# Optimization experiments

Hardware: AMD Instinct MI355X
Metric: run time of the kernel (lower is better)

Reference implementation:

```python
import jax, jax.numpy as jnp
import numpy as np

B, T, C = 4, 4096, 1024
NH, DH = 16, 128          # n_head, d_head = d_qkv // n_head
DQKV, DR = 2048, 256      # d_qkv, d_rank


def _uniform(key, shape, bound):
    return jax.random.uniform(key, shape, jnp.float32, -bound, bound)


def setup_inputs() -> dict:
    key = jax.random.key(0)
    k0, k1, k2, k3, k4 = jax.random.split(key, 5)
    # CastedLinear init: bound = sqrt(3) * 0.5 * in_features**-0.5 (same for w1, w2)
    b_qkv = (3 ** 0.5) * 0.5 * C ** (-0.5)
    b_proj = (3 ** 0.5) * 0.5 * DQKV ** (-0.5)
    return {
        "x": jax.random.normal(k0, (B, T, C), jnp.float32),
        "qkv_w1": _uniform(k1, (DR, C), b_qkv),
        "qkv_w2": _uniform(k2, (3 * DQKV, DR), b_qkv),
        "cproj_w1": _uniform(k3, (DR, DQKV), b_proj),
        "cproj_w2": _uniform(k4, (2 * C, DR), b_proj),
    }


def _rmsnorm(x):
    eps = jnp.finfo(x.dtype).eps  # F.rms_norm default eps
    return x * jax.lax.rsqrt(jnp.mean(x * x, axis=-1, keepdims=True) + eps)


def reference(x, qkv_w1, qkv_w2, cproj_w1, cproj_w2):
    Bx, Tx, Cx = x.shape
    # qkv projection with low-rank factorization + relu^2 activation between factors
    h = _rmsnorm(x) @ qkv_w1.T                      # [B,T,DR]
    h = jnp.square(jax.nn.relu(h))
    qkv = (h @ qkv_w2.T).reshape(Bx, Tx, 3 * NH, DH)
    q, k, v = jnp.split(qkv, 3, axis=2)             # each [B,T,NH,DH]
    q, k = _rmsnorm(q), _rmsnorm(k)

    # rotary embedding: half the head dim rotated, second quarter frequencies zero
    quarter = DH // 4
    freq = (1.0 / 1024.0) ** jnp.linspace(0.0, 1.0, quarter)
    freq = jnp.concatenate([freq, jnp.zeros(quarter, freq.dtype)])  # [DH//2]
    theta = jnp.arange(Tx, dtype=jnp.float32)[:, None] * freq[None, :]
    cos = jnp.cos(theta)[None, :, None, :]          # [1,T,1,DH//2]
    sin = jnp.sin(theta)[None, :, None, :]

    def rope(z):
        z1, z2 = jnp.split(z, 2, axis=-1)
        return jnp.concatenate([z1 * cos + z2 * sin, -z1 * sin + z2 * cos], axis=-1)

    q, k = rope(q), rope(k)

    # causal linear attention: sigmoid-gated cumulative sum over time
    y = jax.nn.relu(q) * jnp.cumsum(jax.nn.sigmoid(k) * v, axis=1)  # [B,T,NH,DH]
    y = y.reshape(Bx, Tx, NH * DH)

    # low-rank output projection (no activation), gated residual
    uv = (y @ cproj_w1.T) @ cproj_w2.T              # [B,T,2C]
    u, g = jnp.split(uv, 2, axis=-1)
    return x + u * jax.nn.silu(g)
```

## Files before the change

### kernel.cpp

```cpp
#include <hip/hip_runtime.h>
#include <hip/hip_bf16.h>

#define TB 4
#define TT 4096
#define TC 1024
#define TNH 16
#define TDH 128
#define TDQKV 2048
#define TDR 256
#define RB 4096
#define ROWS (TB*TT)
#define SLAB (RB*128)
#define NSEG 128
#define SEGT 32

typedef __attribute__((ext_vector_type(8))) short bfx8;
typedef __attribute__((ext_vector_type(4))) float fx4;
typedef __attribute__((address_space(1))) const unsigned char GAS;
typedef __attribute__((address_space(3))) unsigned char LAS;

__device__ __forceinline__ unsigned short f2b(float f) {
    unsigned int u = __float_as_uint(f);
    unsigned int r = (u + 0x7fffu + ((u >> 16) & 1u)) >> 16;
    return (unsigned short)r;
}
__device__ __forceinline__ float b2f(unsigned short h) {
    return __uint_as_float(((unsigned int)h) << 16);
}
__device__ __forceinline__ float sigm(float x) {
    return 1.0f / (1.0f + __expf(-x));
}
__device__ __forceinline__ int xcd_swz(int hw, int nwg) {
    int q = nwg >> 3;
    return (hw & 7) * q + (hw >> 3);
}

__global__ __launch_bounds__(256) void setup_all(const float* __restrict__ wq1, unsigned short* __restrict__ w1b,
                                                 const float* __restrict__ wq2, unsigned short* __restrict__ w2b,
                                                 const float* __restrict__ wc1, unsigned short* __restrict__ wp1b,
                                                 const float* __restrict__ wc2, unsigned short* __restrict__ wp2b,
                                                 float* __restrict__ ct, float* __restrict__ st) {
    int blk = blockIdx.x;
    if (blk < 2816) {
        const float* in; unsigned short* out; int base;
        if (blk < 256)       { in = wq1; out = w1b;  base = blk; }
        else if (blk < 1792) { in = wq2; out = w2b;  base = blk - 256; }
        else if (blk < 2304) { in = wc1; out = wp1b; base = blk - 1792; }
        else                 { in = wc2; out = wp2b; base = blk - 2304; }
        int i = (base * 256 + threadIdx.x) * 4;
        float4 v = *(const float4*)(in + i);
        out[i + 0] = f2b(v.x);
        out[i + 1] = f2b(v.y);
        out[i + 2] = f2b(v.z);
        out[i + 3] = f2b(v.w);
    } else {
        int i = (blk - 2816) * 256 + threadIdx.x;
        int t = i >> 5, j = i & 31;
        float fr = exp2f(-10.0f * (float)j / 31.0f);
        float th = (float)t * fr;
        ct[i] = cosf(th);
        st[i] = sinf(th);
    }
}

__global__ __launch_bounds__(256) void rmsnorm_x(const float* __restrict__ x,
                                                 unsigned short* __restrict__ xn) {
    int row = blockIdx.x;
    int tid = threadIdx.x;
    float4 v = *(const float4*)(x + (size_t)row * TC + tid * 4);
    float ss = v.x * v.x + v.y * v.y + v.z * v.z + v.w * v.w;
    #pragma unroll
    for (int o = 32; o > 0; o >>= 1) ss += __shfl_xor(ss, o);
    __shared__ float red[4];
    if ((tid & 63) == 0) red[tid >> 6] = ss;
    __syncthreads();
    float tot = red[0] + red[1] + red[2] + red[3];
    float sc = rsqrtf(tot * (1.0f / TC) + 1.1920929e-7f);
    unsigned short* o = xn + (size_t)row * TC + tid * 4;
    o[0] = f2b(v.x * sc); o[1] = f2b(v.y * sc); o[2] = f2b(v.z * sc); o[3] = f2b(v.w * sc);
}

template <int EPI>
__global__ __launch_bounds__(256) void gemm_bt(const unsigned short* __restrict__ A, int lda,
                                               const unsigned short* __restrict__ Bm,
                                               unsigned short* __restrict__ C, int ldc,
                                               int N, int K) {
    __shared__ unsigned short As[2][128 * 32];
    __shared__ unsigned short Bs[2][128 * 32];
    const int m0 = blockIdx.y * 128;
    const int n0 = blockIdx.x * 128;
    const int tid = threadIdx.x;
    const int lane = tid & 63;
    const int w = tid >> 6;
    const int wr = w >> 1, wc = w & 1;
    const int r16 = lane & 15;
    const int kk = (lane >> 4) * 8;
    const int l4 = lane >> 2;
    const int c8 = (lane & 3) * 8;
    const int nk = K >> 5;
    fx4 acc[4][4] = {};

    auto stage = [&](int buf, int k0) {
        #pragma unroll
        for (int i = 0; i < 2; ++i) {
            int rr = (w + 4 * i) * 16 + l4;
            const unsigned short* ga = A + (size_t)(m0 + rr) * lda + k0 + c8;
            const unsigned short* gb = Bm + (size_t)(n0 + rr) * K + k0 + c8;
            __builtin_amdgcn_global_load_lds((GAS*)ga, (LAS*)&As[buf][(w + 4 * i) * 512], 16, 0, 0);
            __builtin_amdgcn_global_load_lds((GAS*)gb, (LAS*)&Bs[buf][(w + 4 * i) * 512], 16, 0, 0);
        }
    };

    stage(0, 0);
    __syncthreads();
    int buf = 0;
    for (int ks = 0; ks < nk; ++ks) {
        if (ks + 1 < nk) stage(buf ^ 1, (ks + 1) * 32);
        bfx8 af[4], bfr[4];
        #pragma unroll
        for (int mi = 0; mi < 4; mi++) af[mi] = *(const bfx8*)&As[buf][(wr * 64 + mi * 16 + r16) * 32 + kk];
        #pragma unroll
        for (int ni = 0; ni < 4; ni++) bfr[ni] = *(const bfx8*)&Bs[buf][(wc * 64 + ni * 16 + r16) * 32 + kk];
        #pragma unroll
        for (int mi = 0; mi < 4; mi++)
            #pragma unroll
            for (int ni = 0; ni < 4; ni++)
                acc[mi][ni] = __builtin_amdgcn_mfma_f32_16x16x32_bf16(af[mi], bfr[ni], acc[mi][ni], 0, 0, 0);
        __syncthreads();
        buf ^= 1;
    }

    const int rg = lane >> 4;
    #pragma unroll
    for (int mi = 0; mi < 4; mi++)
        #pragma unroll
        for (int ni = 0; ni < 4; ni++) {
            int col = n0 + wc * 64 + ni * 16 + r16;
            #pragma unroll
            for (int r = 0; r < 4; r++) {
                int row = m0 + wr * 64 + mi * 16 + rg * 4 + r;
                float v = acc[mi][ni][r];
                if (EPI == 1) { v = fmaxf(v, 0.0f); v *= v; }
                if (EPI == 2) {
                    int head = col >> 7;
                    C[(size_t)head * SLAB + (size_t)row * 128 + (col & 127)] = f2b(v);
                } else {
                    C[(size_t)row * ldc + col] = f2b(v);
                }
            }
        }
}

template <int EPI, int NX>
__global__ __launch_bounds__(256) void gemm_sk(const unsigned short* __restrict__ A, int lda,
                                               const unsigned short* __restrict__ Bm,
                                               unsigned short* __restrict__ C, int ldc,
                                               int K) {
    __shared__ unsigned short As[2][128 * 32];
    __shared__ unsigned short Bs[2][64 * 32];
    const int lg = xcd_swz(blockIdx.x, gridDim.x);
    const int n0 = (lg % NX) * 64;
    const int m0 = (lg / NX) * 128;
    const int tid = threadIdx.x;
    const int lane = tid & 63;
    const int w = tid >> 6;
    const int wr = w >> 1, wc = w & 1;
    const int r16 = lane & 15;
    const int kk = (lane >> 4) * 8;
    const int l4 = lane >> 2;
    const int c8 = (lane & 3) * 8;
    const int nk = K >> 5;
    fx4 acc[4][2] = {};

    auto stage = [&](int buf, int k0) {
        #pragma unroll
        for (int i = 0; i < 2; ++i) {
            int rr = (w + 4 * i) * 16 + l4;
            const unsigned short* ga = A + (size_t)(m0 + rr) * lda + k0 + c8;
            __builtin_amdgcn_global_load_lds((GAS*)ga, (LAS*)&As[buf][(w + 4 * i) * 512], 16, 0, 0);
        }
        const unsigned short* gb = Bm + (size_t)(n0 + w * 16 + l4) * K + k0 + c8;
        __builtin_amdgcn_global_load_lds((GAS*)gb, (LAS*)&Bs[buf][w * 512], 16, 0, 0);
    };

    stage(0, 0);
    __syncthreads();
    int buf = 0;
    for (int ks = 0; ks < nk; ++ks) {
        if (ks + 1 < nk) stage(buf ^ 1, (ks + 1) * 32);
        bfx8 af[4], bfr[2];
        #pragma unroll
        for (int mi = 0; mi < 4; mi++) af[mi] = *(const bfx8*)&As[buf][(wr * 64 + mi * 16 + r16) * 32 + kk];
        #pragma unroll
        for (int ni = 0; ni < 2; ni++) bfr[ni] = *(const bfx8*)&Bs[buf][(wc * 32 + ni * 16 + r16) * 32 + kk];
        #pragma unroll
        for (int mi = 0; mi < 4; mi++)
            #pragma unroll
            for (int ni = 0; ni < 2; ni++)
                acc[mi][ni] = __builtin_amdgcn_mfma_f32_16x16x32_bf16(af[mi], bfr[ni], acc[mi][ni], 0, 0, 0);
        __syncthreads();
        buf ^= 1;
    }

    const int rg = lane >> 4;
    #pragma unroll
    for (int mi = 0; mi < 4; mi++)
        #pragma unroll
        for (int ni = 0; ni < 2; ni++) {
            int col = n0 + wc * 32 + ni * 16 + r16;
            #pragma unroll
            for (int r = 0; r < 4; r++) {
                int row = m0 + wr * 64 + mi * 16 + rg * 4 + r;
                float v = acc[mi][ni][r];
                if (EPI == 1) { v = fmaxf(v, 0.0f); v *= v; }
                C[(size_t)row * ldc + col] = f2b(v);
            }
        }
}

__global__ __launch_bounds__(256) void gemm4f64(const unsigned short* __restrict__ A,
                                                const unsigned short* __restrict__ Wm,
                                                const float* __restrict__ x,
                                                float* __restrict__ out) {
    __shared__ unsigned short As[2][64 * 32];
    __shared__ unsigned short Bu[2][64 * 32];
    __shared__ unsigned short Bg[2][64 * 32];
    const int hw = blockIdx.y * gridDim.x + blockIdx.x;
    const int lg = xcd_swz(hw, gridDim.x * gridDim.y);
    const int n0 = (lg & 15) * 64;
    const int m0 = (lg >> 4) * 64;
    const int tid = threadIdx.x;
    const int lane = tid & 63;
    const int w = tid >> 6;
    const int wr = w >> 1, wc = w & 1;
    const int r16 = lane & 15;
    const int rg = lane >> 4;
    const int kk = rg * 8;
    const int l4 = lane >> 2;
    const int c8 = (lane & 3) * 8;
    fx4 accu[2][2] = {};
    fx4 accg[2][2] = {};

    auto stage = [&](int buf, int k0) {
        int rr = w * 16 + l4;
        const unsigned short* ga = A + (size_t)(m0 + rr) * TDR + k0 + c8;
        const unsigned short* gu = Wm + (size_t)(n0 + rr) * TDR + k0 + c8;
        const unsigned short* gg = Wm + (size_t)(1024 + n0 + rr) * TDR + k0 + c8;
        __builtin_amdgcn_global_load_lds((GAS*)ga, (LAS*)&As[buf][w * 512], 16, 0, 0);
        __builtin_amdgcn_global_load_lds((GAS*)gu, (LAS*)&Bu[buf][w * 512], 16, 0, 0);
        __builtin_amdgcn_global_load_lds((GAS*)gg, (LAS*)&Bg[buf][w * 512], 16, 0, 0);
    };

    stage(0, 0);
    float xr[2][2][4];
    #pragma unroll
    for (int mi = 0; mi < 2; mi++)
        #pragma unroll
        for (int ni = 0; ni < 2; ni++)
            #pragma unroll
            for (int r = 0; r < 4; r++)
                xr[mi][ni][r] = x[(size_t)(m0 + wr * 32 + mi * 16 + rg * 4 + r) * TC
                                  + n0 + wc * 32 + ni * 16 + r16];
    __syncthreads();
    int buf = 0;
    for (int ks = 0; ks < 8; ++ks) {
        if (ks + 1 < 8) stage(buf ^ 1, (ks + 1) * 32);
        bfx8 af[2], bu[2], bg[2];
        #pragma unroll
        for (int mi = 0; mi < 2; mi++) af[mi] = *(const bfx8*)&As[buf][(wr * 32 + mi * 16 + r16) * 32 + kk];
        #pragma unroll
        for (int ni = 0; ni < 2; ni++) {
            bu[ni] = *(const bfx8*)&Bu[buf][(wc * 32 + ni * 16 + r16) * 32 + kk];
            bg[ni] = *(const bfx8*)&Bg[buf][(wc * 32 + ni * 16 + r16) * 32 + kk];
        }
        #pragma unroll
        for (int mi = 0; mi < 2; mi++)
            #pragma unroll
            for (int ni = 0; ni < 2; ni++) {
                accu[mi][ni] = __builtin_amdgcn_mfma_f32_16x16x32_bf16(af[mi], bu[ni], accu[mi][ni], 0, 0, 0);
                accg[mi][ni] = __builtin_amdgcn_mfma_f32_16x16x32_bf16(af[mi], bg[ni], accg[mi][ni], 0, 0, 0);
            }
        __syncthreads();
        buf ^= 1;
    }

    #pragma unroll
    for (int mi = 0; mi < 2; mi++)
        #pragma unroll
        for (int ni = 0; ni < 2; ni++) {
            int col = n0 + wc * 32 + ni * 16 + r16;
            #pragma unroll
            for (int r = 0; r < 4; r++) {
                int row = m0 + wr * 32 + mi * 16 + rg * 4 + r;
                float u = accu[mi][ni][r];
                float g = accg[mi][ni][r];
                out[(size_t)row * TC + col] = xr[mi][ni][r] + u * (g * sigm(g));
            }
        }
}

__global__ __launch_bounds__(256) void post64(unsigned short* __restrict__ qkv,
                                              const float* __restrict__ ct,
                                              const float* __restrict__ st,
                                              float* __restrict__ part) {
    const int blk = blockIdx.x;
    const int tile = blk & 63, h = blk >> 6;
    const int g = threadIdx.x >> 4, l16 = threadIdx.x & 15;
    const int d0 = l16 * 4;
    unsigned short* qs = qkv + (size_t)h * SLAB;
    unsigned short* ks = qkv + (size_t)(16 + h) * SLAB;
    unsigned short* vs = qkv + (size_t)(32 + h) * SLAB;
    __shared__ float psum[2][16][128];
    float acc0[2][4] = {};
    float acc1[2][4] = {};

    #pragma unroll
    for (int p = 0; p < 4; ++p) {
        const int t = tile * 64 + p * 16 + g;
        const size_t lo = (size_t)t * 128 + d0, hi = lo + 64;
        ushort4 q1 = *(const ushort4*)(qs + lo);
        ushort4 q2 = *(const ushort4*)(qs + hi);
        ushort4 k1 = *(const ushort4*)(ks + lo);
        ushort4 k2 = *(const ushort4*)(ks + hi);
        float qa[8] = {b2f(q1.x), b2f(q1.y), b2f(q1.z), b2f(q1.w),
                       b2f(q2.x), b2f(q2.y), b2f(q2.z), b2f(q2.w)};
        float ka[8] = {b2f(k1.x), b2f(k1.y), b2f(k1.z), b2f(k1.w),
                       b2f(k2.x), b2f(k2.y), b2f(k2.z), b2f(k2.w)};
        float ssq = 0.0f, ssk = 0.0f;
        #pragma unroll
        for (int j = 0; j < 8; ++j) { ssq += qa[j] * qa[j]; ssk += ka[j] * ka[j]; }
        #pragma unroll
        for (int o = 8; o > 0; o >>= 1) {
            ssq += __shfl_xor(ssq, o);
            ssk += __shfl_xor(ssk, o);
        }
        float qsc = rsqrtf(ssq * (1.0f / TDH) + 1.1920929e-7f);
        float ksc = rsqrtf(ssk * (1.0f / TDH) + 1.1920929e-7f);
        float c[4], s[4];
        if (l16 < 8) {
            float4 cv = *(const float4*)(ct + t * 32 + d0);
            float4 sv = *(const float4*)(st + t * 32 + d0);
            c[0] = cv.x; c[1] = cv.y; c[2] = cv.z; c[3] = cv.w;
            s[0] = sv.x; s[1] = sv.y; s[2] = sv.z; s[3] = sv.w;
        } else {
            c[0] = c[1] = c[2] = c[3] = 1.0f;
            s[0] = s[1] = s[2] = s[3] = 0.0f;
        }
        ushort4 v1 = *(const ushort4*)(vs + lo);
        ushort4 v2 = *(const ushort4*)(vs + hi);
        float va[8] = {b2f(v1.x), b2f(v1.y), b2f(v1.z), b2f(v1.w),
                       b2f(v2.x), b2f(v2.y), b2f(v2.z), b2f(v2.w)};
        ushort4 qo1, qo2, po1, po2;
        unsigned short* qo1p = (unsigned short*)&qo1;
        unsigned short* qo2p = (unsigned short*)&qo2;
        unsigned short* po1p = (unsigned short*)&po1;
        unsigned short* po2p = (unsigned short*)&po2;
        const int h2 = p >> 1;
        #pragma unroll
        for (int j = 0; j < 4; ++j) {
            float z1q = qa[j] * qsc, z2q = qa[4 + j] * qsc;
            float z1k = ka[j] * ksc, z2k = ka[4 + j] * ksc;
            float qlo = z1q * c[j] + z2q * s[j];
            float qhi = z2q * c[j] - z1q * s[j];
            float klo = z1k * c[j] + z2k * s[j];
            float khi = z2k * c[j] - z1k * s[j];
            float plo = sigm(klo) * va[j];
            float phi = sigm(khi) * va[4 + j];
            qo1p[j] = f2b(qlo); qo2p[j] = f2b(qhi);
            po1p[j] = f2b(plo); po2p[j] = f2b(phi);
            acc0[h2][j] += plo;
            acc1[h2][j] += phi;
        }
        *(ushort4*)(qs + lo) = qo1;
        *(ushort4*)(qs + hi) = qo2;
        *(ushort4*)(ks + lo) = po1;
        *(ushort4*)(ks + hi) = po2;
    }
    #pragma unroll
    for (int h2 = 0; h2 < 2; ++h2) {
        *(float4*)&psum[h2][g][d0]      = *(float4*)acc0[h2];
        *(float4*)&psum[h2][g][64 + d0] = *(float4*)acc1[h2];
    }
    __syncthreads();
    const int h2 = threadIdx.x >> 7, d = threadIdx.x & 127;
    float tot = 0.0f;
    #pragma unroll
    for (int gg = 0; gg < 16; ++gg) tot += psum[h2][gg][d];
    part[((size_t)h * NSEG + tile * 2 + h2) * 128 + d] = tot;
}

__global__ __launch_bounds__(256) void scanB128(float* __restrict__ part) {
    int idx = blockIdx.x * 256 + threadIdx.x;
    int h = idx >> 7, d = idx & 127;
    float run = 0.0f;
    #pragma unroll 8
    for (int s = 0; s < NSEG; ++s) {
        float* p = part + ((size_t)(h * NSEG + s)) * 128 + d;
        float tv = *p;
        *p = run;
        run += tv;
    }
}

__global__ __launch_bounds__(256) void scanC3(const unsigned short* __restrict__ qkv,
                                              const float* __restrict__ part,
                                              unsigned short* __restrict__ y) {
    const int bseg = blockIdx.x & 7, h = blockIdx.x >> 3;
    const int g = threadIdx.x >> 4, l16 = threadIdx.x & 15;
    const int seg = bseg * 16 + g;
    const int d0 = l16 * 8;
    const unsigned short* qp = qkv + (size_t)h * SLAB;
    const unsigned short* pp = qkv + (size_t)(16 + h) * SLAB;
    float sum[8];
    const float* pb = part + ((size_t)(h * NSEG + seg)) * 128 + d0;
    *(float4*)&sum[0] = *(const float4*)pb;
    *(float4*)&sum[4] = *(const float4*)(pb + 4);
    #pragma unroll 4
    for (int i = 0; i < SEGT; ++i) {
        int t = seg * SEGT + i;
        size_t off = (size_t)t * 128 + d0;
        bfx8 pv = *(const bfx8*)(pp + off);
        bfx8 qv = *(const bfx8*)(qp + off);
        bfx8 ov;
        #pragma unroll
        for (int j = 0; j < 8; ++j) {
            sum[j] += b2f((unsigned short)pv[j]);
            float q = b2f((unsigned short)qv[j]);
            ov[j] = (short)f2b(fmaxf(q, 0.0f) * sum[j]);
        }
        *(bfx8*)(y + (size_t)t * 2048 + h * 128 + d0) = ov;
    }
}

extern "C" void kernel_launch(void* const* d_in, const int* in_sizes, int n_in,
                              void* d_out, int out_size, void* d_ws, size_t ws_size,
                              hipStream_t stream) {
    (void)in_sizes; (void)n_in; (void)out_size; (void)ws_size;
    const float* x    = (const float*)d_in[0];
    const float* wq1  = (const float*)d_in[1];
    const float* wq2  = (const float*)d_in[2];
    const float* wc1  = (const float*)d_in[3];
    const float* wc2  = (const float*)d_in[4];
    float* out = (float*)d_out;

    char* ws = (char*)d_ws;
    size_t off = 0;
    auto alloc = [&](size_t bytes) -> void* {
        off = (off + 255) & ~(size_t)255;
        void* p = ws + off;
        off += bytes;
        return p;
    };
    char* pool = (char*)alloc((size_t)RB * 6144 * 2);
    unsigned short* qkvb = (unsigned short*)pool;
    unsigned short* xn   = (unsigned short*)pool;
    unsigned short* t1   = (unsigned short*)pool;
    unsigned short* hbuf = (unsigned short*)alloc((size_t)ROWS * TDR * 2);
    unsigned short* w1b  = (unsigned short*)alloc((size_t)TDR * TC * 2);
    unsigned short* w2b  = (unsigned short*)alloc((size_t)3 * TDQKV * TDR * 2);
    unsigned short* wp1b = (unsigned short*)alloc((size_t)TDR * TDQKV * 2);
    unsigned short* wp2b = (unsigned short*)alloc((size_t)2 * TC * TDR * 2);
    float* ct   = (float*)alloc((size_t)TT * 32 * 4);
    float* st   = (float*)alloc((size_t)TT * 32 * 4);
    float* part = (float*)alloc((size_t)TNH * NSEG * 128 * 4);
    unsigned short* ybuf = (unsigned short*)d_out;

    setup_all<<<3328, 256, 0, stream>>>(wq1, w1b, wq2, w2b, wc1, wp1b, wc2, wp2b, ct, st);

    rmsnorm_x<<<ROWS, 256, 0, stream>>>(x, xn);
    gemm_sk<1, 4><<<(ROWS / 128) * (TDR / 64), 256, 0, stream>>>(
        xn, TC, w1b, hbuf, TDR, TC);

    for (int b = 0; b < TB; ++b) {
        gemm_bt<2><<<dim3(6144 / 128, RB / 128), 256, 0, stream>>>(
            hbuf + (size_t)b * RB * TDR, TDR, w2b, qkvb, 0, 6144, TDR);
        post64<<<TNH * 64, 256, 0, stream>>>(qkvb, ct, st, part);
        scanB128<<<(TNH * 128) / 256, 256, 0, stream>>>(part);
        scanC3<<<TNH * 8, 256, 0, stream>>>(qkvb, part, ybuf + (size_t)b * RB * 2048);
    }

    gemm_sk<0, 4><<<(ROWS / 128) * (TDR / 64), 256, 0, stream>>>(
        ybuf, 2048, wp1b, t1, TDR, TDQKV);
    gemm4f64<<<dim3(TC / 64, ROWS / 64), 256, 0, stream>>>(t1, wp2b, x, out);
}
```

Baseline: 376.9 us.

## Fuse qkv GEMM with rmsnorm/rope/sigmoid epilogue and enlarge output GEMM tile

Replaces the generic qkv GEMM and the separate post-processing kernel with one kernel. Each block computes a 64-row tile for one head across its q, k and v sections, then applies q/k rmsnorm, rotary, the sigmoid gate, bf16 stores and segment partial sums in registers. This removes the bf16 round trip of q/k/v through memory and one launch per batch, at the cost of 24 accumulators per wave and a fixed 64x384 tile. The final gated-residual GEMM also moves to 128-row tiles and reads x directly in its epilogue.

```diff
diff --git a/kernel.cpp b/kernel.cpp
--- a/kernel.cpp
+++ b/kernel.cpp
@@ -80,77 +80,6 @@
     o[0] = f2b(v.x * sc); o[1] = f2b(v.y * sc); o[2] = f2b(v.z * sc); o[3] = f2b(v.w * sc);
 }
 
-template <int EPI>
-__global__ __launch_bounds__(256) void gemm_bt(const unsigned short* __restrict__ A, int lda,
-                                               const unsigned short* __restrict__ Bm,
-                                               unsigned short* __restrict__ C, int ldc,
-                                               int N, int K) {
-    __shared__ unsigned short As[2][128 * 32];
-    __shared__ unsigned short Bs[2][128 * 32];
-    const int m0 = blockIdx.y * 128;
-    const int n0 = blockIdx.x * 128;
-    const int tid = threadIdx.x;
-    const int lane = tid & 63;
-    const int w = tid >> 6;
-    const int wr = w >> 1, wc = w & 1;
-    const int r16 = lane & 15;
-    const int kk = (lane >> 4) * 8;
-    const int l4 = lane >> 2;
-    const int c8 = (lane & 3) * 8;
-    const int nk = K >> 5;
-    fx4 acc[4][4] = {};
-
-    auto stage = [&](int buf, int k0) {
-        #pragma unroll
-        for (int i = 0; i < 2; ++i) {
-            int rr = (w + 4 * i) * 16 + l4;
-            const unsigned short* ga = A + (size_t)(m0 + rr) * lda + k0 + c8;
-            const unsigned short* gb = Bm + (size_t)(n0 + rr) * K + k0 + c8;
-            __builtin_amdgcn_global_load_lds((GAS*)ga, (LAS*)&As[buf][(w + 4 * i) * 512], 16, 0, 0);
-            __builtin_amdgcn_global_load_lds((GAS*)gb, (LAS*)&Bs[buf][(w + 4 * i) * 512], 16, 0, 0);
-        }
-    };
-
-    stage(0, 0);
-    __syncthreads();
-    int buf = 0;
-    for (int ks = 0; ks < nk; ++ks) {
-        if (ks + 1 < nk) stage(buf ^ 1, (ks + 1) * 32);
-        bfx8 af[4], bfr[4];
-        #pragma unroll
-        for (int mi = 0; mi < 4; mi++) af[mi] = *(const bfx8*)&As[buf][(wr * 64 + mi * 16 + r16) * 32 + kk];
-        #pragma unroll
-        for (int ni = 0; ni < 4; ni++) bfr[ni] = *(const bfx8*)&Bs[buf][(wc * 64 + ni * 16 + r16) * 32 + kk];
-        #pragma unroll
-        for (int mi = 0; mi < 4; mi++)
-            #pragma unroll
-            for (int ni = 0; ni < 4; ni++)
-                acc[mi][ni] = __builtin_amdgcn_mfma_f32_16x16x32_bf16(af[mi], bfr[ni], acc[mi][ni], 0, 0, 0);
-        __syncthreads();
-        buf ^= 1;
-    }
-
-    const int rg = lane >> 4;
-    #pragma unroll
-    for (int mi = 0; mi < 4; mi++)
-        #pragma unroll
-        for (int ni = 0; ni < 4; ni++) {
-            int col = n0 + wc * 64 + ni * 16 + r16;
-            #pragma unroll
-            for (int r = 0; r < 4; r++) {
-                int row = m0 + wr * 64 + mi * 16 + rg * 4 + r;
-                float v = acc[mi][ni][r];
-                if (EPI == 1) { v = fmaxf(v, 0.0f); v *= v; }
-                if (EPI == 2) {
-                    int head = col >> 7;
-                    C[(size_t)head * SLAB + (size_t)row * 128 + (col & 127)] = f2b(v);
-                } else {
-                    C[(size_t)row * ldc + col] = f2b(v);
-                }
-            }
-        }
-}
-
 template <int EPI, int NX>
 __global__ __launch_bounds__(256) void gemm_sk(const unsigned short* __restrict__ A, int lda,
                                                const unsigned short* __restrict__ Bm,
@@ -218,17 +147,116 @@
         }
 }
 
-__global__ __launch_bounds__(256) void gemm4f64(const unsigned short* __restrict__ A,
-                                                const unsigned short* __restrict__ Wm,
-                                                const float* __restrict__ x,
-                                                float* __restrict__ out) {
+__global__ __launch_bounds__(256) void gemm2f(const unsigned short* __restrict__ A,
+                                              const unsigned short* __restrict__ W,
+                                              unsigned short* __restrict__ qkv,
+                                              const float* __restrict__ ct,
+                                              const float* __restrict__ st,
+                                              float* __restrict__ part) {
     __shared__ unsigned short As[2][64 * 32];
+    __shared__ unsigned short Bs[2][384 * 32];
+    __shared__ float psum[4][128];
+    const int lg = xcd_swz(blockIdx.x, 1024);
+    const int h = lg >> 6, mb = lg & 63;
+    const int m0 = mb * 64;
+    const int tid = threadIdx.x;
+    const int lane = tid & 63;
+    const int w = tid >> 6;
+    const int r16 = lane & 15;
+    const int rg = lane >> 4;
+    const int kk = rg * 8;
+    const int l4 = lane >> 2;
+    const int c8 = (lane & 3) * 8;
+    const int sec0 = h * 128, sec1 = 2048 + h * 128, sec2 = 4096 + h * 128;
+    fx4 acc[24] = {};
+
+    auto stage = [&](int buf, int k0) {
+        __builtin_amdgcn_global_load_lds((GAS*)(A + (size_t)(m0 + w * 16 + l4) * TDR + k0 + c8),
+                                         (LAS*)&As[buf][w * 512], 16, 0, 0);
+        #pragma unroll
+        for (int i = 0; i < 6; ++i) {
+            int c = w + 4 * i;
+            int sec = c >> 3;
+            int grow = (sec == 0 ? sec0 : (sec == 1 ? sec1 : sec2)) + (c & 7) * 16 + l4;
+            __builtin_amdgcn_global_load_lds((GAS*)(W + (size_t)grow * TDR + k0 + c8),
+                                             (LAS*)&Bs[buf][c * 512], 16, 0, 0);
+        }
+    };
+
+    stage(0, 0);
+    __syncthreads();
+    int buf = 0;
+    for (int ks = 0; ks < 8; ++ks) {
+        if (ks + 1 < 8) stage(buf ^ 1, (ks + 1) * 32);
+        bfx8 af = *(const bfx8*)&As[buf][(w * 16 + r16) * 32 + kk];
+        #pragma unroll
+        for (int ni = 0; ni < 24; ++ni) {
+            bfx8 bb = *(const bfx8*)&Bs[buf][(ni * 16 + r16) * 32 + kk];
+            acc[ni] = __builtin_amdgcn_mfma_f32_16x16x32_bf16(af, bb, acc[ni], 0, 0, 0);
+        }
+        __syncthreads();
+        buf ^= 1;
+    }
+
+    unsigned short* qs = qkv + (size_t)h * SLAB;
+    unsigned short* ps = qkv + (size_t)(16 + h) * SLAB;
+    float pseg[8] = {};
+    #pragma unroll
+    for (int r = 0; r < 4; ++r) {
+        int t = m0 + w * 16 + rg * 4 + r;
+        float ssq = 0.0f, ssk = 0.0f;
+        #pragma unroll
+        for (int ni = 0; ni < 8; ++ni) {
+            ssq += acc[ni][r] * acc[ni][r];
+            ssk += acc[8 + ni][r] * acc[8 + ni][r];
+        }
+        #pragma unroll
+        for (int o = 1; o < 16; o <<= 1) { ssq += __shfl_xor(ssq, o); ssk += __shfl_xor(ssk, o); }
+        float qsc = rsqrtf(ssq * (1.0f / TDH) + 1.1920929e-7f);
+        float ksc = rsqrtf(ssk * (1.0f / TDH) + 1.1920929e-7f);
+        #pragma unroll
+        for (int j = 0; j < 4; ++j) {
+            int d = j * 16 + r16;
+            float c = 1.0f, s = 0.0f;
+            if (j < 2) { c = ct[t * 32 + d]; s = st[t * 32 + d]; }
+            float z1q = acc[j][r] * qsc,      z2q = acc[j + 4][r] * qsc;
+            float z1k = acc[8 + j][r] * ksc,  z2k = acc[12 + j][r] * ksc;
+            float qlo = z1q * c + z2q * s, qhi = z2q * c - z1q * s;
+            float klo = z1k * c + z2k * s, khi = z2k * c - z1k * s;
+            float plo = sigm(klo) * acc[16 + j][r];
+            float phi = sigm(khi) * acc[20 + j][r];
+            qs[(size_t)t * 128 + d]      = f2b(qlo);
+            qs[(size_t)t * 128 + 64 + d] = f2b(qhi);
+            ps[(size_t)t * 128 + d]      = f2b(plo);
+            ps[(size_t)t * 128 + 64 + d] = f2b(phi);
+            pseg[j] += plo;
+            pseg[j + 4] += phi;
+        }
+    }
+    #pragma unroll
+    for (int j = 0; j < 8; ++j) {
+        pseg[j] += __shfl_xor(pseg[j], 16);
+        pseg[j] += __shfl_xor(pseg[j], 32);
+    }
+    if (lane < 16) {
+        #pragma unroll
+        for (int j = 0; j < 8; ++j) psum[w][j * 16 + lane] = pseg[j];
+    }
+    __syncthreads();
+    int sg = tid >> 7, d = tid & 127;
+    part[((size_t)h * NSEG + mb * 2 + sg) * 128 + d] = psum[sg * 2][d] + psum[sg * 2 + 1][d];
+}
+
+__global__ __launch_bounds__(256) void gemm4f128(const unsigned short* __restrict__ A,
+                                                 const unsigned short* __restrict__ Wm,
+                                                 const float* __restrict__ x,
+                                                 float* __restrict__ out) {
+    __shared__ unsigned short As[2][128 * 32];
     __shared__ unsigned short Bu[2][64 * 32];
     __shared__ unsigned short Bg[2][64 * 32];
-    const int hw = blockIdx.y * gridDim.x + blockIdx.x;
-    const int lg = xcd_swz(hw, gridDim.x * gridDim.y);
+    const int lg = xcd_swz(blockIdx.x, gridDim.x);
     const int n0 = (lg & 15) * 64;
-    const int m0 = (lg >> 4) * 64;
+    const int m0 = (lg >> 4) * 128;
     const int tid = threadIdx.x;
     const int lane = tid & 63;
     const int w = tid >> 6;
@@ -238,43 +266,38 @@
     const int kk = rg * 8;
     const int l4 = lane >> 2;
     const int c8 = (lane & 3) * 8;
-    fx4 accu[2][2] = {};
-    fx4 accg[2][2] = {};
+    fx4 accu[4][2] = {};
+    fx4 accg[4][2] = {};
 
     auto stage = [&](int buf, int k0) {
+        #pragma unroll
+        for (int i = 0; i < 2; ++i) {
+            int rr = (w + 4 * i) * 16 + l4;
+            __builtin_amdgcn_global_load_lds((GAS*)(A + (size_t)(m0 + rr) * TDR + k0 + c8),
+                                             (LAS*)&As[buf][(w + 4 * i) * 512], 16, 0, 0);
+        }
         int rr = w * 16 + l4;
-        const unsigned short* ga = A + (size_t)(m0 + rr) * TDR + k0 + c8;
-        const unsigned short* gu = Wm + (size_t)(n0 + rr) * TDR + k0 + c8;
-        const unsigned short* gg = Wm + (size_t)(1024 + n0 + rr) * TDR + k0 + c8;
-        __builtin_amdgcn_global_load_lds((GAS*)ga, (LAS*)&As[buf][w * 512], 16, 0, 0);
-        __builtin_amdgcn_global_load_lds((GAS*)gu, (LAS*)&Bu[buf][w * 512], 16, 0, 0);
-        __builtin_amdgcn_global_load_lds((GAS*)gg, (LAS*)&Bg[buf][w * 512], 16, 0, 0);
+        __builtin_amdgcn_global_load_lds((GAS*)(Wm + (size_t)(n0 + rr) * TDR + k0 + c8),
+                                         (LAS*)&Bu[buf][w * 512], 16, 0, 0);
+        __builtin_amdgcn_global_load_lds((GAS*)(Wm + (size_t)(1024 + n0 + rr) * TDR + k0 + c8),
+                                         (LAS*)&Bg[buf][w * 512], 16, 0, 0);
     };
 
     stage(0, 0);
-    float xr[2][2][4];
-    #pragma unroll
-    for (int mi = 0; mi < 2; mi++)
-        #pragma unroll
-        for (int ni = 0; ni < 2; ni++)
-            #pragma unroll
-            for (int r = 0; r < 4; r++)
-                xr[mi][ni][r] = x[(size_t)(m0 + wr * 32 + mi * 16 + rg * 4 + r) * TC
-                                  + n0 + wc * 32 + ni * 16 + r16];
     __syncthreads();
     int buf = 0;
     for (int ks = 0; ks < 8; ++ks) {
         if (ks + 1 < 8) stage(buf ^ 1, (ks + 1) * 32);
-        bfx8 af[2], bu[2], bg[2];
-        #pragma unroll
-        for (int mi = 0; mi < 2; mi++) af[mi] = *(const bfx8*)&As[buf][(wr * 32 + mi * 16 + r16) * 32 + kk];
+        bfx8 af[4], bu[2], bg[2];
+        #pragma unroll
+        for (int mi = 0; mi < 4; mi++) af[mi] = *(const bfx8*)&As[buf][(wr * 64 + mi * 16 + r16) * 32 + kk];
         #pragma unroll
         for (int ni = 0; ni < 2; ni++) {
             bu[ni] = *(const bfx8*)&Bu[buf][(wc * 32 + ni * 16 + r16) * 32 + kk];
             bg[ni] = *(const bfx8*)&Bg[buf][(wc * 32 + ni * 16 + r16) * 32 + kk];
         }
         #pragma unroll
-        for (int mi = 0; mi < 2; mi++)
+        for (int mi = 0; mi < 4; mi++)
             #pragma unroll
             for (int ni = 0; ni < 2; ni++) {
                 accu[mi][ni] = __builtin_amdgcn_mfma_f32_16x16x32_bf16(af[mi], bu[ni], accu[mi][ni], 0, 0, 0);
@@ -285,108 +308,19 @@
     }
 
     #pragma unroll
-    for (int mi = 0; mi < 2; mi++)
+    for (int mi = 0; mi < 4; mi++)
         #pragma unroll
         for (int ni = 0; ni < 2; ni++) {
             int col = n0 + wc * 32 + ni * 16 + r16;
             #pragma unroll
             for (int r = 0; r < 4; r++) {
-                int row = m0 + wr * 32 + mi * 16 + rg * 4 + r;
+                int row = m0 + wr * 64 + mi * 16 + rg * 4 + r;
                 float u = accu[mi][ni][r];
                 float g = accg[mi][ni][r];
-                out[(size_t)row * TC + col] = xr[mi][ni][r] + u * (g * sigm(g));
+                size_t idx = (size_t)row * TC + col;
+                out[idx] = x[idx] + u * (g * sigm(g));
             }
         }
-}
-
-__global__ __launch_bounds__(256) void post64(unsigned short* __restrict__ qkv,
-                                              const float* __restrict__ ct,
-                                              const float* __restrict__ st,
-                                              float* __restrict__ part) {
-    const int blk = blockIdx.x;
-    const int tile = blk & 63, h = blk >> 6;
-    const int g = threadIdx.x >> 4, l16 = threadIdx.x & 15;
-    const int d0 = l16 * 4;
-    unsigned short* qs = qkv + (size_t)h * SLAB;
-    unsigned short* ks = qkv + (size_t)(16 + h) * SLAB;
-    unsigned short* vs = qkv + (size_t)(32 + h) * SLAB;
-    __shared__ float psum[2][16][128];
-    float acc0[2][4] = {};
-    float acc1[2][4] = {};
-
-    #pragma unroll
-    for (int p = 0; p < 4; ++p) {
-        const int t = tile * 64 + p * 16 + g;
-        const size_t lo = (size_t)t * 128 + d0, hi = lo + 64;
-        ushort4 q1 = *(const ushort4*)(qs + lo);
-        ushort4 q2 = *(const ushort4*)(qs + hi);
-        ushort4 k1 = *(const ushort4*)(ks + lo);
-        ushort4 k2 = *(const ushort4*)(ks + hi);
-        float qa[8] = {b2f(q1.x), b2f(q1.y), b2f(q1.z), b2f(q1.w),
-                       b2f(q2.x), b2f(q2.y), b2f(q2.z), b2f(q2.w)};
-        float ka[8] = {b2f(k1.x), b2f(k1.y), b2f(k1.z), b2f(k1.w),
-                       b2f(k2.x), b2f(k2.y), b2f(k2.z), b2f(k2.w)};
-        float ssq = 0.0f, ssk = 0.0f;
-        #pragma unroll
-        for (int j = 0; j < 8; ++j) { ssq += qa[j] * qa[j]; ssk += ka[j] * ka[j]; }
-        #pragma unroll
-        for (int o = 8; o > 0; o >>= 1) {
-            ssq += __shfl_xor(ssq, o);
-            ssk += __shfl_xor(ssk, o);
-        }
-        float qsc = rsqrtf(ssq * (1.0f / TDH) + 1.1920929e-7f);
-        float ksc = rsqrtf(ssk * (1.0f / TDH) + 1.1920929e-7f);
-        float c[4], s[4];
-        if (l16 < 8) {
-            float4 cv = *(const float4*)(ct + t * 32 + d0);
-            float4 sv = *(const float4*)(st + t * 32 + d0);
-            c[0] = cv.x; c[1] = cv.y; c[2] = cv.z; c[3] = cv.w;
-            s[0] = sv.x; s[1] = sv.y; s[2] = sv.z; s[3] = sv.w;
-        } else {
-            c[0] = c[1] = c[2] = c[3] = 1.0f;
-            s[0] = s[1] = s[2] = s[3] = 0.0f;
-        }
-        ushort4 v1 = *(const ushort4*)(vs + lo);
-        ushort4 v2 = *(const ushort4*)(vs + hi);
-        float va[8] = {b2f(v1.x), b2f(v1.y), b2f(v1.z), b2f(v1.w),
-                       b2f(v2.x), b2f(v2.y), b2f(v2.z), b2f(v2.w)};
-        ushort4 qo1, qo2, po1, po2;
-        unsigned short* qo1p = (unsigned short*)&qo1;
-        unsigned short* qo2p = (unsigned short*)&qo2;
-        unsigned short* po1p = (unsigned short*)&po1;
-        unsigned short* po2p = (unsigned short*)&po2;
-        const int h2 = p >> 1;
-        #pragma unroll
-        for (int j = 0; j < 4; ++j) {
-            float z1q = qa[j] * qsc, z2q = qa[4 + j] * qsc;
-            float z1k = ka[j] * ksc, z2k = ka[4 + j] * ksc;
-            float qlo = z1q * c[j] + z2q * s[j];
-            float qhi = z2q * c[j] - z1q * s[j];
-            float klo = z1k * c[j] + z2k * s[j];
-            float khi = z2k * c[j] - z1k * s[j];
-            float plo = sigm(klo) * va[j];
-            float phi = sigm(khi) * va[4 + j];
-            qo1p[j] = f2b(qlo); qo2p[j] = f2b(qhi);
-            po1p[j] = f2b(plo); po2p[j] = f2b(phi);
-            acc0[h2][j] += plo;
-            acc1[h2][j] += phi;
-        }
-        *(ushort4*)(qs + lo) = qo1;
-        *(ushort4*)(qs + hi) = qo2;
-        *(ushort4*)(ks + lo) = po1;
-        *(ushort4*)(ks + hi) = po2;
-    }
-    #pragma unroll
-    for (int h2 = 0; h2 < 2; ++h2) {
-        *(float4*)&psum[h2][g][d0]      = *(float4*)acc0[h2];
-        *(float4*)&psum[h2][g][64 + d0] = *(float4*)acc1[h2];
-    }
-    __syncthreads();
-    const int h2 = threadIdx.x >> 7, d = threadIdx.x & 127;
-    float tot = 0.0f;
-    #pragma unroll
-    for (int gg = 0; gg < 16; ++gg) tot += psum[h2][gg][d];
-    part[((size_t)h * NSEG + tile * 2 + h2) * 128 + d] = tot;
 }
 
 __global__ __launch_bounds__(256) void scanB128(float* __restrict__ part) {
@@ -451,7 +385,7 @@
         off += bytes;
         return p;
     };
-    char* pool = (char*)alloc((size_t)RB * 6144 * 2);
+    char* pool = (char*)alloc((size_t)RB * 4096 * 2);
     unsigned short* qkvb = (unsigned short*)pool;
     unsigned short* xn   = (unsigned short*)pool;
     unsigned short* t1   = (unsigned short*)pool;
@@ -472,14 +406,13 @@
         xn, TC, w1b, hbuf, TDR, TC);
 
     for (int b = 0; b < TB; ++b) {
-        gemm_bt<2><<<dim3(6144 / 128, RB / 128), 256, 0, stream>>>(
-            hbuf + (size_t)b * RB * TDR, TDR, w2b, qkvb, 0, 6144, TDR);
-        post64<<<TNH * 64, 256, 0, stream>>>(qkvb, ct, st, part);
+        gemm2f<<<1024, 256, 0, stream>>>(
+            hbuf + (size_t)b * RB * TDR, w2b, qkvb, ct, st, part);
         scanB128<<<(TNH * 128) / 256, 256, 0, stream>>>(part);
         scanC3<<<TNH * 8, 256, 0, stream>>>(qkvb, part, ybuf + (size_t)b * RB * 2048);
     }
 
     gemm_sk<0, 4><<<(ROWS / 128) * (TDR / 64), 256, 0, stream>>>(
         ybuf, 2048, wp1b, t1, TDR, TDQKV);
-    gemm4f64<<<dim3(TC / 64, ROWS / 64), 256, 0, stream>>>(t1, wp2b, x, out);
-}
+    gemm4f128<<<(ROWS / 128) * (TC / 64), 256, 0, stream>>>(t1, wp2b, x, out);
+}
```

New measurement: 576.2 us. 52.9% more time.

## Move q norm/rope into scan kernel, widen final GEMM tile to 128 rows

Applied to the files above, without the earlier changes.

The post kernel now handles only k normalisation, rope and the sigmoid-gated product, with 8-wide vector loads and a shuffle for the rotated half. The q rmsnorm and rope move into the scan consumer kernel, which now launches more, smaller blocks. This removes the q write-back and reread, at the cost of recomputing the q norm inside the sequential scan loop. The final gated-residual GEMM switches to 128x64 tiles on a 1-D swizzled grid to reuse the weight tiles more, and reads x in the epilogue instead of prefetching it.

```diff
diff --git a/kernel.cpp b/kernel.cpp
--- a/kernel.cpp
+++ b/kernel.cpp
@@ -218,17 +218,16 @@
         }
 }
 
-__global__ __launch_bounds__(256) void gemm4f64(const unsigned short* __restrict__ A,
-                                                const unsigned short* __restrict__ Wm,
-                                                const float* __restrict__ x,
-                                                float* __restrict__ out) {
-    __shared__ unsigned short As[2][64 * 32];
+__global__ __launch_bounds__(256) void gemm4f128(const unsigned short* __restrict__ A,
+                                                 const unsigned short* __restrict__ Wm,
+                                                 const float* __restrict__ x,
+                                                 float* __restrict__ out) {
+    __shared__ unsigned short As[2][128 * 32];
     __shared__ unsigned short Bu[2][64 * 32];
     __shared__ unsigned short Bg[2][64 * 32];
-    const int hw = blockIdx.y * gridDim.x + blockIdx.x;
-    const int lg = xcd_swz(hw, gridDim.x * gridDim.y);
+    const int lg = xcd_swz(blockIdx.x, gridDim.x);
     const int n0 = (lg & 15) * 64;
-    const int m0 = (lg >> 4) * 64;
+    const int m0 = (lg >> 4) * 128;
     const int tid = threadIdx.x;
     const int lane = tid & 63;
     const int w = tid >> 6;
@@ -238,43 +237,38 @@
     const int kk = rg * 8;
     const int l4 = lane >> 2;
     const int c8 = (lane & 3) * 8;
-    fx4 accu[2][2] = {};
-    fx4 accg[2][2] = {};
+    fx4 accu[4][2] = {};
+    fx4 accg[4][2] = {};
 
     auto stage = [&](int buf, int k0) {
+        #pragma unroll
+        for (int i = 0; i < 2; ++i) {
+            int rr = (w + 4 * i) * 16 + l4;
+            __builtin_amdgcn_global_load_lds((GAS*)(A + (size_t)(m0 + rr) * TDR + k0 + c8),
+                                             (LAS*)&As[buf][(w + 4 * i) * 512], 16, 0, 0);
+        }
         int rr = w * 16 + l4;
-        const unsigned short* ga = A + (size_t)(m0 + rr) * TDR + k0 + c8;
-        const unsigned short* gu = Wm + (size_t)(n0 + rr) * TDR + k0 + c8;
-        const unsigned short* gg = Wm + (size_t)(1024 + n0 + rr) * TDR + k0 + c8;
-        __builtin_amdgcn_global_load_lds((GAS*)ga, (LAS*)&As[buf][w * 512], 16, 0, 0);
-        __builtin_amdgcn_global_load_lds((GAS*)gu, (LAS*)&Bu[buf][w * 512], 16, 0, 0);
-        __builtin_amdgcn_global_load_lds((GAS*)gg, (LAS*)&Bg[buf][w * 512], 16, 0, 0);
+        __builtin_amdgcn_global_load_lds((GAS*)(Wm + (size_t)(n0 + rr) * TDR + k0 + c8),
+                                         (LAS*)&Bu[buf][w * 512], 16, 0, 0);
+        __builtin_amdgcn_global_load_lds((GAS*)(Wm + (size_t)(1024 + n0 + rr) * TDR + k0 + c8),
+                                         (LAS*)&Bg[buf][w * 512], 16, 0, 0);
     };
 
     stage(0, 0);
-    float xr[2][2][4];
-    #pragma unroll
-    for (int mi = 0; mi < 2; mi++)
-        #pragma unroll
-        for (int ni = 0; ni < 2; ni++)
-            #pragma unroll
-            for (int r = 0; r < 4; r++)
-                xr[mi][ni][r] = x[(size_t)(m0 + wr * 32 + mi * 16 + rg * 4 + r) * TC
-                                  + n0 + wc * 32 + ni * 16 + r16];
     __syncthreads();
     int buf = 0;
     for (int ks = 0; ks < 8; ++ks) {
         if (ks + 1 < 8) stage(buf ^ 1, (ks + 1) * 32);
-        bfx8 af[2], bu[2], bg[2];
-        #pragma unroll
-        for (int mi = 0; mi < 2; mi++) af[mi] = *(const bfx8*)&As[buf][(wr * 32 + mi * 16 + r16) * 32 + kk];
+        bfx8 af[4], bu[2], bg[2];
+        #pragma unroll
+        for (int mi = 0; mi < 4; mi++) af[mi] = *(const bfx8*)&As[buf][(wr * 64 + mi * 16 + r16) * 32 + kk];
         #pragma unroll
         for (int ni = 0; ni < 2; ni++) {
             bu[ni] = *(const bfx8*)&Bu[buf][(wc * 32 + ni * 16 + r16) * 32 + kk];
             bg[ni] = *(const bfx8*)&Bg[buf][(wc * 32 + ni * 16 + r16) * 32 + kk];
         }
         #pragma unroll
-        for (int mi = 0; mi < 2; mi++)
+        for (int mi = 0; mi < 4; mi++)
             #pragma unroll
             for (int ni = 0; ni < 2; ni++) {
                 accu[mi][ni] = __builtin_amdgcn_mfma_f32_16x16x32_bf16(af[mi], bu[ni], accu[mi][ni], 0, 0, 0);
@@ -285,102 +279,83 @@
     }
 
     #pragma unroll
-    for (int mi = 0; mi < 2; mi++)
+    for (int mi = 0; mi < 4; mi++)
         #pragma unroll
         for (int ni = 0; ni < 2; ni++) {
             int col = n0 + wc * 32 + ni * 16 + r16;
             #pragma unroll
             for (int r = 0; r < 4; r++) {
-                int row = m0 + wr * 32 + mi * 16 + rg * 4 + r;
+                int row = m0 + wr * 64 + mi * 16 + rg * 4 + r;
                 float u = accu[mi][ni][r];
                 float g = accg[mi][ni][r];
-                out[(size_t)row * TC + col] = xr[mi][ni][r] + u * (g * sigm(g));
+                size_t idx = (size_t)row * TC + col;
+                out[idx] = x[idx] + u * (g * sigm(g));
             }
         }
 }
 
-__global__ __launch_bounds__(256) void post64(unsigned short* __restrict__ qkv,
+__global__ __launch_bounds__(256) void postKV(unsigned short* __restrict__ qkv,
                                               const float* __restrict__ ct,
                                               const float* __restrict__ st,
                                               float* __restrict__ part) {
-    const int blk = blockIdx.x;
-    const int tile = blk & 63, h = blk >> 6;
+    const int tile = blockIdx.x & 63, h = blockIdx.x >> 6;
     const int g = threadIdx.x >> 4, l16 = threadIdx.x & 15;
-    const int d0 = l16 * 4;
-    unsigned short* qs = qkv + (size_t)h * SLAB;
+    const int d0 = l16 * 8;
+    const int dl = (l16 & 7) * 8;
+    const bool rot = dl < 32;
+    const float se = (l16 < 8) ? 1.0f : -1.0f;
     unsigned short* ks = qkv + (size_t)(16 + h) * SLAB;
-    unsigned short* vs = qkv + (size_t)(32 + h) * SLAB;
+    const unsigned short* vs = qkv + (size_t)(32 + h) * SLAB;
     __shared__ float psum[2][16][128];
-    float acc0[2][4] = {};
-    float acc1[2][4] = {};
-
-    #pragma unroll
-    for (int p = 0; p < 4; ++p) {
-        const int t = tile * 64 + p * 16 + g;
-        const size_t lo = (size_t)t * 128 + d0, hi = lo + 64;
-        ushort4 q1 = *(const ushort4*)(qs + lo);
-        ushort4 q2 = *(const ushort4*)(qs + hi);
-        ushort4 k1 = *(const ushort4*)(ks + lo);
-        ushort4 k2 = *(const ushort4*)(ks + hi);
-        float qa[8] = {b2f(q1.x), b2f(q1.y), b2f(q1.z), b2f(q1.w),
-                       b2f(q2.x), b2f(q2.y), b2f(q2.z), b2f(q2.w)};
-        float ka[8] = {b2f(k1.x), b2f(k1.y), b2f(k1.z), b2f(k1.w),
-                       b2f(k2.x), b2f(k2.y), b2f(k2.z), b2f(k2.w)};
-        float ssq = 0.0f, ssk = 0.0f;
-        #pragma unroll
-        for (int j = 0; j < 8; ++j) { ssq += qa[j] * qa[j]; ssk += ka[j] * ka[j]; }
-        #pragma unroll
-        for (int o = 8; o > 0; o >>= 1) {
-            ssq += __shfl_xor(ssq, o);
-            ssk += __shfl_xor(ssk, o);
-        }
-        float qsc = rsqrtf(ssq * (1.0f / TDH) + 1.1920929e-7f);
+    float acc[2][8] = {};
+
+    #pragma unroll
+    for (int p4 = 0; p4 < 4; ++p4) {
+        const int t = tile * 64 + p4 * 16 + g;
+        const size_t off = (size_t)t * 128 + d0;
+        bfx8 k8 = *(const bfx8*)(ks + off);
+        float ka[8];
+        #pragma unroll
+        for (int j = 0; j < 8; ++j) ka[j] = b2f((unsigned short)k8[j]);
+        float ssk = 0.0f;
+        #pragma unroll
+        for (int j = 0; j < 8; ++j) ssk += ka[j] * ka[j];
+        #pragma unroll
+        for (int o = 1; o < 16; o <<= 1) ssk += __shfl_xor(ssk, o);
         float ksc = rsqrtf(ssk * (1.0f / TDH) + 1.1920929e-7f);
-        float c[4], s[4];
-        if (l16 < 8) {
-            float4 cv = *(const float4*)(ct + t * 32 + d0);
-            float4 sv = *(const float4*)(st + t * 32 + d0);
-            c[0] = cv.x; c[1] = cv.y; c[2] = cv.z; c[3] = cv.w;
-            s[0] = sv.x; s[1] = sv.y; s[2] = sv.z; s[3] = sv.w;
+        #pragma unroll
+        for (int j = 0; j < 8; ++j) ka[j] *= ksc;
+        float kb[8];
+        #pragma unroll
+        for (int j = 0; j < 8; ++j) kb[j] = __shfl_xor(ka[j], 8);
+        float c[8], s[8];
+        if (rot) {
+            float4 c0 = *(const float4*)(ct + t * 32 + dl);
+            float4 c1 = *(const float4*)(ct + t * 32 + dl + 4);
+            float4 s0 = *(const float4*)(st + t * 32 + dl);
+            float4 s1 = *(const float4*)(st + t * 32 + dl + 4);
+            c[0]=c0.x; c[1]=c0.y; c[2]=c0.z; c[3]=c0.w; c[4]=c1.x; c[5]=c1.y; c[6]=c1.z; c[7]=c1.w;
+            s[0]=s0.x; s[1]=s0.y; s[2]=s0.z; s[3]=s0.w; s[4]=s1.x; s[5]=s1.y; s[6]=s1.z; s[7]=s1.w;
         } else {
-            c[0] = c[1] = c[2] = c[3] = 1.0f;
-            s[0] = s[1] = s[2] = s[3] = 0.0f;
-        }
-        ushort4 v1 = *(const ushort4*)(vs + lo);
-        ushort4 v2 = *(const ushort4*)(vs + hi);
-        float va[8] = {b2f(v1.x), b2f(v1.y), b2f(v1.z), b2f(v1.w),
-                       b2f(v2.x), b2f(v2.y), b2f(v2.z), b2f(v2.w)};
-        ushort4 qo1, qo2, po1, po2;
-        unsigned short* qo1p = (unsigned short*)&qo1;
-        unsigned short* qo2p = (unsigned short*)&qo2;
-        unsigned short* po1p = (unsigned short*)&po1;
-        unsigned short* po2p = (unsigned short*)&po2;
-        const int h2 = p >> 1;
-        #pragma unroll
-        for (int j = 0; j < 4; ++j) {
-            float z1q = qa[j] * qsc, z2q = qa[4 + j] * qsc;
-            float z1k = ka[j] * ksc, z2k = ka[4 + j] * ksc;
-            float qlo = z1q * c[j] + z2q * s[j];
-            float qhi = z2q * c[j] - z1q * s[j];
-            float klo = z1k * c[j] + z2k * s[j];
-            float khi = z2k * c[j] - z1k * s[j];
-            float plo = sigm(klo) * va[j];
-            float phi = sigm(khi) * va[4 + j];
-            qo1p[j] = f2b(qlo); qo2p[j] = f2b(qhi);
-            po1p[j] = f2b(plo); po2p[j] = f2b(phi);
-            acc0[h2][j] += plo;
-            acc1[h2][j] += phi;
-        }
-        *(ushort4*)(qs + lo) = qo1;
-        *(ushort4*)(qs + hi) = qo2;
-        *(ushort4*)(ks + lo) = po1;
-        *(ushort4*)(ks + hi) = po2;
-    }
-    #pragma unroll
-    for (int h2 = 0; h2 < 2; ++h2) {
-        *(float4*)&psum[h2][g][d0]      = *(float4*)acc0[h2];
-        *(float4*)&psum[h2][g][64 + d0] = *(float4*)acc1[h2];
-    }
+            #pragma unroll
+            for (int j = 0; j < 8; ++j) { c[j] = 1.0f; s[j] = 0.0f; }
+        }
+        bfx8 v8 = *(const bfx8*)(vs + off);
+        bfx8 po;
+        const int h2 = p4 >> 1;
+        #pragma unroll
+        for (int j = 0; j < 8; ++j) {
+            float kr = ka[j] * c[j] + kb[j] * (s[j] * se);
+            float p = sigm(kr) * b2f((unsigned short)v8[j]);
+            po[j] = (short)f2b(p);
+            acc[h2][j] += p;
+        }
+        *(bfx8*)(ks + off) = po;
+    }
+    #pragma unroll
+    for (int h2 = 0; h2 < 2; ++h2)
+        #pragma unroll
+        for (int j = 0; j < 8; ++j) psum[h2][g][d0 + j] = acc[h2][j];
     __syncthreads();
     const int h2 = threadIdx.x >> 7, d = threadIdx.x & 127;
     float tot = 0.0f;
@@ -402,31 +377,61 @@
     }
 }
 
-__global__ __launch_bounds__(256) void scanC3(const unsigned short* __restrict__ qkv,
-                                              const float* __restrict__ part,
-                                              unsigned short* __restrict__ y) {
-    const int bseg = blockIdx.x & 7, h = blockIdx.x >> 3;
+__global__ __launch_bounds__(64) void scanCQ(const unsigned short* __restrict__ qkv,
+                                             const float* __restrict__ part,
+                                             unsigned short* __restrict__ y,
+                                             const float* __restrict__ ct,
+                                             const float* __restrict__ st) {
+    const int bseg = blockIdx.x & 31, h = blockIdx.x >> 5;
     const int g = threadIdx.x >> 4, l16 = threadIdx.x & 15;
-    const int seg = bseg * 16 + g;
+    const int seg = bseg * 4 + g;
     const int d0 = l16 * 8;
+    const int dl = (l16 & 7) * 8;
+    const bool rot = dl < 32;
+    const float se = (l16 < 8) ? 1.0f : -1.0f;
     const unsigned short* qp = qkv + (size_t)h * SLAB;
     const unsigned short* pp = qkv + (size_t)(16 + h) * SLAB;
     float sum[8];
     const float* pb = part + ((size_t)(h * NSEG + seg)) * 128 + d0;
     *(float4*)&sum[0] = *(const float4*)pb;
     *(float4*)&sum[4] = *(const float4*)(pb + 4);
-    #pragma unroll 4
     for (int i = 0; i < SEGT; ++i) {
-        int t = seg * SEGT + i;
-        size_t off = (size_t)t * 128 + d0;
-        bfx8 pv = *(const bfx8*)(pp + off);
-        bfx8 qv = *(const bfx8*)(qp + off);
+        const int t = seg * SEGT + i;
+        const size_t off = (size_t)t * 128 + d0;
+        bfx8 p8 = *(const bfx8*)(pp + off);
+        bfx8 q8 = *(const bfx8*)(qp + off);
+        float qa[8];
+        #pragma unroll
+        for (int j = 0; j < 8; ++j) qa[j] = b2f((unsigned short)q8[j]);
+        float ssq = 0.0f;
+        #pragma unroll
+        for (int j = 0; j < 8; ++j) ssq += qa[j] * qa[j];
+        #pragma unroll
+        for (int o = 1; o < 16; o <<= 1) ssq += __shfl_xor(ssq, o);
+        float qsc = rsqrtf(ssq * (1.0f / TDH) + 1.1920929e-7f);
+        #pragma unroll
+        for (int j = 0; j < 8; ++j) qa[j] *= qsc;
+        float qb[8];
+        #pragma unroll
+        for (int j = 0; j < 8; ++j) qb[j] = __shfl_xor(qa[j], 8);
+        float c[8], s[8];
+        if (rot) {
+            float4 c0 = *(const float4*)(ct + t * 32 + dl);
+            float4 c1 = *(const float4*)(ct + t * 32 + dl + 4);
+            float4 s0 = *(const float4*)(st + t * 32 + dl);
+            float4 s1 = *(const float4*)(st + t * 32 + dl + 4);
+            c[0]=c0.x; c[1]=c0.y; c[2]=c0.z; c[3]=c0.w; c[4]=c1.x; c[5]=c1.y; c[6]=c1.z; c[7]=c1.w;
+            s[0]=s0.x; s[1]=s0.y; s[2]=s0.z; s[3]=s0.w; s[4]=s1.x; s[5]=s1.y; s[6]=s1.z; s[7]=s1.w;
+        } else {
+            #pragma unroll
+            for (int j = 0; j < 8; ++j) { c[j] = 1.0f; s[j] = 0.0f; }
+        }
         bfx8 ov;
         #pragma unroll
         for (int j = 0; j < 8; ++j) {
-            sum[j] += b2f((unsigned short)pv[j]);
-            float q = b2f((unsigned short)qv[j]);
-            ov[j] = (short)f2b(fmaxf(q, 0.0f) * sum[j]);
+            float qr = qa[j] * c[j] + qb[j] * (s[j] * se);
+            sum[j] += b2f((unsigned short)p8[j]);
+            ov[j] = (short)f2b(fmaxf(qr, 0.0f) * sum[j]);
         }
         *(bfx8*)(y + (size_t)t * 2048 + h * 128 + d0) = ov;
     }
@@ -474,12 +479,12 @@
     for (int b = 0; b < TB; ++b) {
         gemm_bt<2><<<dim3(6144 / 128, RB / 128), 256, 0, stream>>>(
             hbuf + (size_t)b * RB * TDR, TDR, w2b, qkvb, 0, 6144, TDR);
-        post64<<<TNH * 64, 256, 0, stream>>>(qkvb, ct, st, part);
+        postKV<<<TNH * 64, 256, 0, stream>>>(qkvb, ct, st, part);
         scanB128<<<(TNH * 128) / 256, 256, 0, stream>>>(part);
-        scanC3<<<TNH * 8, 256, 0, stream>>>(qkvb, part, ybuf + (size_t)b * RB * 2048);
+        scanCQ<<<TNH * 32, 64, 0, stream>>>(qkvb, part, ybuf + (size_t)b * RB * 2048, ct, st);
     }
 
     gemm_sk<0, 4><<<(ROWS / 128) * (TDR / 64), 256, 0, stream>>>(
         ybuf, 2048, wp1b, t1, TDR, TDQKV);
-    gemm4f64<<<dim3(TC / 64, ROWS / 64), 256, 0, stream>>>(t1, wp2b, x, out);
-}
+    gemm4f128<<<(ROWS / 128) * (TC / 64), 256, 0, stream>>>(t1, wp2b, x, out);
+}
```

Result: slower. 427.8 us (+13.5%).
